# Kernel optimization log

Hardware: AMD Instinct MI355X
Metric: run time of the kernel (lower is better)

## Reference

```python
import jax, jax.numpy as jnp
import numpy as np

B = 65536
H = W = 28
K = 3
OUT_HW = H - K + 1  # 26, valid conv
FEAT = OUT_HW * OUT_HW  # 676
HID = 200
NCLS = 10


def setup_inputs() -> dict:
    key = jax.random.key(0)
    ks = jax.random.split(key, 6)
    x = jax.random.normal(ks[0], (B, H * W), dtype=jnp.float32)
    conv_w = jnp.ones((K, K), dtype=jnp.float32)  # Parameter(ones((3,3)))
    w1 = jax.random.normal(ks[1], (FEAT, HID), dtype=jnp.float32) * (1.0 / np.sqrt(FEAT))
    b1 = jnp.zeros((HID,), dtype=jnp.float32)
    w2 = jax.random.normal(ks[2], (HID, NCLS), dtype=jnp.float32) * (1.0 / np.sqrt(HID))
    b2 = jnp.zeros((NCLS,), dtype=jnp.float32)
    return {"x": x, "conv_w": conv_w, "w1": w1, "b1": b1, "w2": w2, "b2": b2}


def _forward(x, conv_w, w1, b1, w2, b2):
    img = x.reshape(-1, H, W)  # (B,28,28)
    # valid 3x3 single-channel cross-correlation (matches input[i:i+3,j:j+3]*w)
    lhs = img[:, None, :, :]          # (B,1,28,28)
    rhs = conv_w[None, None, :, :]    # (1,1,3,3)
    conv = jax.lax.conv_general_dilated(
        lhs, rhs, window_strides=(1, 1), padding="VALID",
        dimension_numbers=("NCHW", "OIHW", "NCHW"))  # (B,1,26,26)
    feat = conv.reshape(-1, FEAT)     # (B,676)
    hidden = jax.nn.relu(feat @ w1 + b1)  # (B,200)
    return hidden @ w2 + b2               # (B,10) logits


def reference(x, conv_w, w1, b1, w2, b2):
    return _forward(x, conv_w, w1, b1, w2, b2)
```

## Files before the change

### kernel.cpp

```cpp
#include <hip/hip_runtime.h>
#include <hip/hip_bf16.h>

#define BATCH   65536
#define HW      28
#define OHW     26
#define FEAT    676
#define HID     200
#define NCLS    10
#define MT      16
#define NBLOCKS (BATCH / MT)

typedef __attribute__((ext_vector_type(8))) __bf16 bf16x8;
typedef __attribute__((ext_vector_type(4))) float  f32x4;

__device__ __forceinline__ unsigned int pk2(float a, float b) {
  __hip_bfloat16 ha = __float2bfloat16(a), hb = __float2bfloat16(b);
  return (unsigned int)__builtin_bit_cast(unsigned short, ha)
       | ((unsigned int)__builtin_bit_cast(unsigned short, hb) << 16);
}

__device__ __forceinline__ unsigned short* fslot(unsigned short* base, int m, int k) {
  const int kc = k >> 5;
  return base + ((kc * 64 + ((k >> 3) & 3) * 16 + (m ^ (kc & 7))) * 8) + (k & 7);
}

__global__ __launch_bounds__(256) void prep_w1tf(const float* __restrict__ w1,
                                                 unsigned short* __restrict__ w1tf) {
  int idx = blockIdx.x * 256 + threadIdx.x;
  if (idx >= 704 * 208) return;
  int k = idx / 208;
  int n = idx - k * 208;
  float v = (k < FEAT && n < HID) ? w1[k * HID + n] : 0.f;
  int nt = n >> 4, ln = n & 15;
  int kc = k >> 5, r = k & 31, qd = r >> 3, j = r & 7;
  size_t dst = ((size_t)(kc * 13 + nt) * 64 + qd * 16 + ln) * 8 + j;
  __hip_bfloat16 h = __float2bfloat16(v);
  w1tf[dst] = __builtin_bit_cast(unsigned short, h);
}

__global__ __launch_bounds__(256) void prep_w2f(const float* __restrict__ w2,
                                                unsigned short* __restrict__ w2f) {
  int t = blockIdx.x * 256 + threadIdx.x;
  if (t >= 7 * 64 * 8) return;
  int j = t & 7, lane = (t >> 3) & 63, kc = t >> 9;
  int c = lane & 15;
  int k = kc * 32 + (lane >> 4) * 8 + j;
  float v = (c < NCLS && k < HID) ? w2[k * NCLS + c] : 0.f;
  __hip_bfloat16 h = __float2bfloat16(v);
  w2f[t] = __builtin_bit_cast(unsigned short, h);
}

template<int NT0, int NT>
__device__ __forceinline__ void gemm1_slice(
    const unsigned short* featA, const unsigned short* __restrict__ w1tf,
    const float* __restrict__ b1, unsigned short* hidA, int lane) {
  const int ln = lane & 15, qd = lane >> 4;
  f32x4 acc[NT];
  #pragma unroll
  for (int t = 0; t < NT; ++t) acc[t] = (f32x4){0.f, 0.f, 0.f, 0.f};
  for (int kc = 0; kc < 22; ++kc) {
    bf16x8 a = *(const bf16x8*)&featA[(kc * 64 + (lane ^ (kc & 7))) * 8];
    #pragma unroll
    for (int t = 0; t < NT; ++t) {
      bf16x8 b = *(const bf16x8*)(w1tf + ((size_t)(kc * 13 + NT0 + t) * 64 + lane) * 8);
      acc[t] = __builtin_amdgcn_mfma_f32_16x16x32_bf16(a, b, acc[t], 0, 0, 0);
    }
  }
  #pragma unroll
  for (int t = 0; t < NT; ++t) {
    const int n = (NT0 + t) * 16 + ln;
    if (n < HID) {
      const float bias = b1[n];
      const int kc2 = n >> 5, qd2 = (n >> 3) & 3, j2 = n & 7, c2 = kc2 & 7;
      #pragma unroll
      for (int rr = 0; rr < 4; ++rr) {
        const int m = qd * 4 + rr;
        float h = fmaxf(acc[t][rr] + bias, 0.f);
        __hip_bfloat16 hb = __float2bfloat16(h);
        hidA[(kc2 * 64 + qd2 * 16 + (m ^ c2)) * 8 + j2] =
            __builtin_bit_cast(unsigned short, hb);
      }
    }
  }
}

__global__ __launch_bounds__(256, 5) void fused2(
    const float* __restrict__ x, const float* __restrict__ cwp,
    const unsigned short* __restrict__ w1tf, const unsigned short* __restrict__ w2f,
    const float* __restrict__ b1, const float* __restrict__ b2,
    float* __restrict__ out) {
  __shared__ __align__(16) unsigned short featA[22 * 64 * 8];
  __shared__ __align__(16) unsigned short hidA [ 7 * 64 * 8];
  const int tid  = threadIdx.x;
  const int wave = tid >> 6;
  const int lane = tid & 63;

  for (int i = tid; i < MT * 14; i += 256) {
    int m = i / 14, d = i - m * 14;
    *(unsigned int*)fslot(featA, m, 676 + 2 * d) = 0u;
  }
  for (int i = tid; i < MT * 12; i += 256) {
    int m = i / 12, d = i - m * 12;
    *(unsigned int*)fslot(hidA, m, 200 + 2 * d) = 0u;
  }

  float cw[9];
  #pragma unroll
  for (int t = 0; t < 9; ++t) cw[t] = cwp[t];

  const float* xb = x + (size_t)blockIdx.x * (MT * 784);
  for (int t0 = 0; t0 < 364; t0 += 64) {
    const int t = t0 + lane;
    if (t < 364) {
      const int p   = (t * 721) >> 16;
      const int r91 = t - 91 * p;
      const int iq  = (r91 * 9363) >> 16;
      const int jc  = r91 - 7 * iq;
      const int m   = 4 * p + wave;
      const float* xw = xb + m * 784;
      float in[4][6];
      const int c2 = (jc < 6) ? 4 : 2;
      #pragma unroll
      for (int rr = 0; rr < 4; ++rr) {
        const float* rp = xw + (2 * iq + rr) * HW + 4 * jc;
        const float4 v = *(const float4*)rp;
        const float2 u = *(const float2*)(rp + c2);
        in[rr][0] = v.x; in[rr][1] = v.y; in[rr][2] = v.z; in[rr][3] = v.w;
        in[rr][4] = u.x; in[rr][5] = u.y;
      }
      float o[2][4];
      #pragma unroll
      for (int dr = 0; dr < 2; ++dr)
        #pragma unroll
        for (int dc = 0; dc < 4; ++dc) {
          float s = 0.f;
          #pragma unroll
          for (int di = 0; di < 3; ++di)
            #pragma unroll
            for (int dj = 0; dj < 3; ++dj)
              s += cw[di * 3 + dj] * in[dr + di][dc + dj];
          o[dr][dc] = s;
        }
      const int k0 = 52 * iq + 4 * jc;
      if (jc < 6) {
        *(uint2*)fslot(featA, m, k0) =
            make_uint2(pk2(o[0][0], o[0][1]), pk2(o[0][2], o[0][3]));
        *(unsigned int*)fslot(featA, m, k0 + OHW)     = pk2(o[1][0], o[1][1]);
        *(unsigned int*)fslot(featA, m, k0 + OHW + 2) = pk2(o[1][2], o[1][3]);
      } else {
        *(unsigned int*)fslot(featA, m, k0)       = pk2(o[0][0], o[0][1]);
        *(unsigned int*)fslot(featA, m, k0 + OHW) = pk2(o[1][0], o[1][1]);
      }
    }
  }
  __syncthreads();

  switch (wave) {
    case 0:  gemm1_slice<0, 4>(featA, w1tf, b1, hidA, lane); break;
    case 1:  gemm1_slice<4, 3>(featA, w1tf, b1, hidA, lane); break;
    case 2:  gemm1_slice<7, 3>(featA, w1tf, b1, hidA, lane); break;
    default: gemm1_slice<10, 3>(featA, w1tf, b1, hidA, lane); break;
  }
  __syncthreads();

  if (wave == 0) {
    const int ln = lane & 15, qd = lane >> 4;
    f32x4 acc2 = (f32x4){0.f, 0.f, 0.f, 0.f};
    #pragma unroll
    for (int kc = 0; kc < 7; ++kc) {
      bf16x8 a = *(const bf16x8*)&hidA[(kc * 64 + (lane ^ (kc & 7))) * 8];
      bf16x8 b = *(const bf16x8*)(w2f + ((size_t)kc * 64 + lane) * 8);
      acc2 = __builtin_amdgcn_mfma_f32_16x16x32_bf16(a, b, acc2, 0, 0, 0);
    }
    if (ln < NCLS) {
      const float bb = b2[ln];
      #pragma unroll
      for (int rr = 0; rr < 4; ++rr) {
        out[((size_t)blockIdx.x * MT + qd * 4 + rr) * NCLS + ln] = acc2[rr] + bb;
      }
    }
  }
}

extern "C" void kernel_launch(void* const* d_in, const int* in_sizes, int n_in,
                              void* d_out, int out_size, void* d_ws, size_t ws_size,
                              hipStream_t stream) {
  const float* x  = (const float*)d_in[0];
  const float* cw = (const float*)d_in[1];
  const float* w1 = (const float*)d_in[2];
  const float* b1 = (const float*)d_in[3];
  const float* w2 = (const float*)d_in[4];
  const float* b2 = (const float*)d_in[5];
  float* out = (float*)d_out;

  unsigned short* w1tf = (unsigned short*)d_ws;
  unsigned short* w2f  = (unsigned short*)((char*)d_ws + 294912);

  hipLaunchKernelGGL(prep_w1tf, dim3((704 * 208 + 255) / 256), dim3(256), 0, stream,
                     w1, w1tf);
  hipLaunchKernelGGL(prep_w2f, dim3(14), dim3(256), 0, stream, w2, w2f);
  hipLaunchKernelGGL(fused2, dim3(NBLOCKS), dim3(256), 0, stream,
                     x, cw, w1tf, w2f, b1, b2, out);
}
```

Before: 355.4 us.

## Split conv and GEMM into separate kernels with 64-row GEMM tiles

```diff
diff --git a/kernel.cpp b/kernel.cpp
--- a/kernel.cpp
+++ b/kernel.cpp
@@ -9,6 +9,8 @@
 #define NCLS    10
 #define MT      16
 #define NBLOCKS (BATCH / MT)
+#define MT2     64
+#define GBLOCKS (BATCH / MT2)
 
 typedef __attribute__((ext_vector_type(8))) __bf16 bf16x8;
 typedef __attribute__((ext_vector_type(4))) float  f32x4;
@@ -26,71 +28,45 @@
 
 __global__ __launch_bounds__(256) void prep_w1tf(const float* __restrict__ w1,
                                                  unsigned short* __restrict__ w1tf) {
-  int idx = blockIdx.x * 256 + threadIdx.x;
-  if (idx >= 704 * 208) return;
-  int k = idx / 208;
-  int n = idx - k * 208;
-  float v = (k < FEAT && n < HID) ? w1[k * HID + n] : 0.f;
-  int nt = n >> 4, ln = n & 15;
-  int kc = k >> 5, r = k & 31, qd = r >> 3, j = r & 7;
-  size_t dst = ((size_t)(kc * 13 + nt) * 64 + qd * 16 + ln) * 8 + j;
-  __hip_bfloat16 h = __float2bfloat16(v);
-  w1tf[dst] = __builtin_bit_cast(unsigned short, h);
+  int c = blockIdx.x * 256 + threadIdx.x;
+  if (c >= 22 * 13 * 64) return;
+  int ln = c & 15;
+  int qd = (c >> 4) & 3;
+  int g  = c >> 6;
+  int kc = g / 13, nt = g - kc * 13;
+  int n  = nt * 16 + ln;
+  float v[8];
+  #pragma unroll
+  for (int j = 0; j < 8; ++j) {
+    int k = kc * 32 + qd * 8 + j;
+    v[j] = (k < FEAT && n < HID) ? w1[k * HID + n] : 0.f;
+  }
+  uint4 o = make_uint4(pk2(v[0], v[1]), pk2(v[2], v[3]),
+                       pk2(v[4], v[5]), pk2(v[6], v[7]));
+  *(uint4*)(w1tf + (size_t)c * 8) = o;
 }
 
 __global__ __launch_bounds__(256) void prep_w2f(const float* __restrict__ w2,
                                                 unsigned short* __restrict__ w2f) {
-  int t = blockIdx.x * 256 + threadIdx.x;
-  if (t >= 7 * 64 * 8) return;
-  int j = t & 7, lane = (t >> 3) & 63, kc = t >> 9;
-  int c = lane & 15;
-  int k = kc * 32 + (lane >> 4) * 8 + j;
-  float v = (c < NCLS && k < HID) ? w2[k * NCLS + c] : 0.f;
-  __hip_bfloat16 h = __float2bfloat16(v);
-  w2f[t] = __builtin_bit_cast(unsigned short, h);
-}
-
-template<int NT0, int NT>
-__device__ __forceinline__ void gemm1_slice(
-    const unsigned short* featA, const unsigned short* __restrict__ w1tf,
-    const float* __restrict__ b1, unsigned short* hidA, int lane) {
-  const int ln = lane & 15, qd = lane >> 4;
-  f32x4 acc[NT];
-  #pragma unroll
-  for (int t = 0; t < NT; ++t) acc[t] = (f32x4){0.f, 0.f, 0.f, 0.f};
-  for (int kc = 0; kc < 22; ++kc) {
-    bf16x8 a = *(const bf16x8*)&featA[(kc * 64 + (lane ^ (kc & 7))) * 8];
-    #pragma unroll
-    for (int t = 0; t < NT; ++t) {
-      bf16x8 b = *(const bf16x8*)(w1tf + ((size_t)(kc * 13 + NT0 + t) * 64 + lane) * 8);
-      acc[t] = __builtin_amdgcn_mfma_f32_16x16x32_bf16(a, b, acc[t], 0, 0, 0);
-    }
-  }
-  #pragma unroll
-  for (int t = 0; t < NT; ++t) {
-    const int n = (NT0 + t) * 16 + ln;
-    if (n < HID) {
-      const float bias = b1[n];
-      const int kc2 = n >> 5, qd2 = (n >> 3) & 3, j2 = n & 7, c2 = kc2 & 7;
-      #pragma unroll
-      for (int rr = 0; rr < 4; ++rr) {
-        const int m = qd * 4 + rr;
-        float h = fmaxf(acc[t][rr] + bias, 0.f);
-        __hip_bfloat16 hb = __float2bfloat16(h);
-        hidA[(kc2 * 64 + qd2 * 16 + (m ^ c2)) * 8 + j2] =
-            __builtin_bit_cast(unsigned short, hb);
-      }
-    }
-  }
-}
-
-__global__ __launch_bounds__(256, 5) void fused2(
-    const float* __restrict__ x, const float* __restrict__ cwp,
-    const unsigned short* __restrict__ w1tf, const unsigned short* __restrict__ w2f,
-    const float* __restrict__ b1, const float* __restrict__ b2,
-    float* __restrict__ out) {
+  int c = blockIdx.x * 256 + threadIdx.x;
+  if (c >= 7 * 64) return;
+  int lane = c & 63, kc = c >> 6;
+  int col = lane & 15;
+  float v[8];
+  #pragma unroll
+  for (int j = 0; j < 8; ++j) {
+    int k = kc * 32 + (lane >> 4) * 8 + j;
+    v[j] = (col < NCLS && k < HID) ? w2[k * NCLS + col] : 0.f;
+  }
+  uint4 o = make_uint4(pk2(v[0], v[1]), pk2(v[2], v[3]),
+                       pk2(v[4], v[5]), pk2(v[6], v[7]));
+  *(uint4*)(w2f + (size_t)c * 8) = o;
+}
+
+__global__ __launch_bounds__(256) void convk(const float* __restrict__ x,
+                                             const float* __restrict__ cwp,
+                                             unsigned short* __restrict__ featg) {
   __shared__ __align__(16) unsigned short featA[22 * 64 * 8];
-  __shared__ __align__(16) unsigned short hidA [ 7 * 64 * 8];
   const int tid  = threadIdx.x;
   const int wave = tid >> 6;
   const int lane = tid & 63;
@@ -98,10 +74,6 @@
   for (int i = tid; i < MT * 14; i += 256) {
     int m = i / 14, d = i - m * 14;
     *(unsigned int*)fslot(featA, m, 676 + 2 * d) = 0u;
-  }
-  for (int i = tid; i < MT * 12; i += 256) {
-    int m = i / 12, d = i - m * 12;
-    *(unsigned int*)fslot(hidA, m, 200 + 2 * d) = 0u;
   }
 
   float cw[9];
@@ -155,6 +127,204 @@
   }
   __syncthreads();
 
+  const uint4* src = (const uint4*)featA;
+  uint4* dst = (uint4*)(featg + (size_t)blockIdx.x * (22 * 64 * 8));
+  for (int i = tid; i < 1408; i += 256) dst[i] = src[i];
+}
+
+template<int NT0, int NT>
+__device__ __forceinline__ void gemmB_slice(
+    const unsigned short* __restrict__ featg, const unsigned short* __restrict__ w1tf,
+    const float* __restrict__ b1, unsigned short* hidA, int lane, int blk4) {
+  const int ln = lane & 15, qd = lane >> 4;
+  f32x4 acc[4][NT];
+  #pragma unroll
+  for (int mi = 0; mi < 4; ++mi)
+    #pragma unroll
+    for (int t = 0; t < NT; ++t) acc[mi][t] = (f32x4){0.f, 0.f, 0.f, 0.f};
+
+  for (int kc = 0; kc < 22; ++kc) {
+    const int sw = lane ^ (kc & 7);
+    bf16x8 b[NT];
+    #pragma unroll
+    for (int t = 0; t < NT; ++t)
+      b[t] = *(const bf16x8*)(w1tf + ((size_t)(kc * 13 + NT0 + t) * 64 + lane) * 8);
+    bf16x8 a[4];
+    #pragma unroll
+    for (int mi = 0; mi < 4; ++mi)
+      a[mi] = *(const bf16x8*)(featg + ((size_t)((blk4 + mi) * 22 + kc) * 64 + sw) * 8);
+    #pragma unroll
+    for (int mi = 0; mi < 4; ++mi)
+      #pragma unroll
+      for (int t = 0; t < NT; ++t)
+        acc[mi][t] = __builtin_amdgcn_mfma_f32_16x16x32_bf16(a[mi], b[t], acc[mi][t], 0, 0, 0);
+  }
+
+  #pragma unroll
+  for (int t = 0; t < NT; ++t) {
+    const int n = (NT0 + t) * 16 + ln;
+    if (n < HID) {
+      const float bias = b1[n];
+      const int kc2 = n >> 5, qd2 = (n >> 3) & 3, j2 = n & 7, c2 = kc2 & 7;
+      #pragma unroll
+      for (int mi = 0; mi < 4; ++mi)
+        #pragma unroll
+        for (int rr = 0; rr < 4; ++rr) {
+          const int m = qd * 4 + rr;
+          float h = fmaxf(acc[mi][t][rr] + bias, 0.f);
+          __hip_bfloat16 hb = __float2bfloat16(h);
+          hidA[mi * 3584 + (kc2 * 64 + qd2 * 16 + (m ^ c2)) * 8 + j2] =
+              __builtin_bit_cast(unsigned short, hb);
+        }
+    }
+  }
+}
+
+__global__ __launch_bounds__(256, 4) void gemmk(
+    const unsigned short* __restrict__ featg, const unsigned short* __restrict__ w1tf,
+    const unsigned short* __restrict__ w2f, const float* __restrict__ b1,
+    const float* __restrict__ b2, float* __restrict__ out) {
+  __shared__ __align__(16) unsigned short hidA[4 * 7 * 64 * 8];
+  const int tid  = threadIdx.x;
+  const int wave = tid >> 6;
+  const int lane = tid & 63;
+
+  for (int i = tid; i < 768; i += 256) {
+    int mi = i / 192, r = i - mi * 192, m = r / 12, d = r - m * 12;
+    *(unsigned int*)fslot(hidA + mi * 3584, m, 200 + 2 * d) = 0u;
+  }
+
+  const int blk4 = blockIdx.x * 4;
+  switch (wave) {
+    case 0:  gemmB_slice<0, 4>(featg, w1tf, b1, hidA, lane, blk4); break;
+    case 1:  gemmB_slice<4, 3>(featg, w1tf, b1, hidA, lane, blk4); break;
+    case 2:  gemmB_slice<7, 3>(featg, w1tf, b1, hidA, lane, blk4); break;
+    default: gemmB_slice<10, 3>(featg, w1tf, b1, hidA, lane, blk4); break;
+  }
+  __syncthreads();
+
+  const int ln = lane & 15, qd = lane >> 4;
+  f32x4 acc2 = (f32x4){0.f, 0.f, 0.f, 0.f};
+  #pragma unroll
+  for (int kc = 0; kc < 7; ++kc) {
+    bf16x8 a = *(const bf16x8*)&hidA[wave * 3584 + (kc * 64 + (lane ^ (kc & 7))) * 8];
+    bf16x8 b = *(const bf16x8*)(w2f + ((size_t)kc * 64 + lane) * 8);
+    acc2 = __builtin_amdgcn_mfma_f32_16x16x32_bf16(a, b, acc2, 0, 0, 0);
+  }
+  if (ln < NCLS) {
+    const float bb = b2[ln];
+    #pragma unroll
+    for (int rr = 0; rr < 4; ++rr) {
+      out[((size_t)(blk4 + wave) * 16 + qd * 4 + rr) * NCLS + ln] = acc2[rr] + bb;
+    }
+  }
+}
+
+template<int NT0, int NT>
+__device__ __forceinline__ void gemm1_slice(
+    const unsigned short* featA, const unsigned short* __restrict__ w1tf,
+    const float* __restrict__ b1, unsigned short* hidA, int lane) {
+  const int ln = lane & 15, qd = lane >> 4;
+  f32x4 acc[NT];
+  #pragma unroll
+  for (int t = 0; t < NT; ++t) acc[t] = (f32x4){0.f, 0.f, 0.f, 0.f};
+  for (int kc = 0; kc < 22; ++kc) {
+    bf16x8 a = *(const bf16x8*)&featA[(kc * 64 + (lane ^ (kc & 7))) * 8];
+    #pragma unroll
+    for (int t = 0; t < NT; ++t) {
+      bf16x8 b = *(const bf16x8*)(w1tf + ((size_t)(kc * 13 + NT0 + t) * 64 + lane) * 8);
+      acc[t] = __builtin_amdgcn_mfma_f32_16x16x32_bf16(a, b, acc[t], 0, 0, 0);
+    }
+  }
+  #pragma unroll
+  for (int t = 0; t < NT; ++t) {
+    const int n = (NT0 + t) * 16 + ln;
+    if (n < HID) {
+      const float bias = b1[n];
+      const int kc2 = n >> 5, qd2 = (n >> 3) & 3, j2 = n & 7, c2 = kc2 & 7;
+      #pragma unroll
+      for (int rr = 0; rr < 4; ++rr) {
+        const int m = qd * 4 + rr;
+        float h = fmaxf(acc[t][rr] + bias, 0.f);
+        __hip_bfloat16 hb = __float2bfloat16(h);
+        hidA[(kc2 * 64 + qd2 * 16 + (m ^ c2)) * 8 + j2] =
+            __builtin_bit_cast(unsigned short, hb);
+      }
+    }
+  }
+}
+
+__global__ __launch_bounds__(256, 5) void fused2(
+    const float* __restrict__ x, const float* __restrict__ cwp,
+    const unsigned short* __restrict__ w1tf, const unsigned short* __restrict__ w2f,
+    const float* __restrict__ b1, const float* __restrict__ b2,
+    float* __restrict__ out) {
+  __shared__ __align__(16) unsigned short featA[22 * 64 * 8];
+  __shared__ __align__(16) unsigned short hidA [ 7 * 64 * 8];
+  const int tid  = threadIdx.x;
+  const int wave = tid >> 6;
+  const int lane = tid & 63;
+
+  for (int i = tid; i < MT * 14; i += 256) {
+    int m = i / 14, d = i - m * 14;
+    *(unsigned int*)fslot(featA, m, 676 + 2 * d) = 0u;
+  }
+  for (int i = tid; i < MT * 12; i += 256) {
+    int m = i / 12, d = i - m * 12;
+    *(unsigned int*)fslot(hidA, m, 200 + 2 * d) = 0u;
+  }
+
+  float cw[9];
+  #pragma unroll
+  for (int t = 0; t < 9; ++t) cw[t] = cwp[t];
+
+  const float* xb = x + (size_t)blockIdx.x * (MT * 784);
+  for (int t0 = 0; t0 < 364; t0 += 64) {
+    const int t = t0 + lane;
+    if (t < 364) {
+      const int p   = (t * 721) >> 16;
+      const int r91 = t - 91 * p;
+      const int iq  = (r91 * 9363) >> 16;
+      const int jc  = r91 - 7 * iq;
+      const int m   = 4 * p + wave;
+      const float* xw = xb + m * 784;
+      float in[4][6];
+      const int c2 = (jc < 6) ? 4 : 2;
+      #pragma unroll
+      for (int rr = 0; rr < 4; ++rr) {
+        const float* rp = xw + (2 * iq + rr) * HW + 4 * jc;
+        const float4 v = *(const float4*)rp;
+        const float2 u = *(const float2*)(rp + c2);
+        in[rr][0] = v.x; in[rr][1] = v.y; in[rr][2] = v.z; in[rr][3] = v.w;
+        in[rr][4] = u.x; in[rr][5] = u.y;
+      }
+      float o[2][4];
+      #pragma unroll
+      for (int dr = 0; dr < 2; ++dr)
+        #pragma unroll
+        for (int dc = 0; dc < 4; ++dc) {
+          float s = 0.f;
+          #pragma unroll
+          for (int di = 0; di < 3; ++di)
+            #pragma unroll
+            for (int dj = 0; dj < 3; ++dj)
+              s += cw[di * 3 + dj] * in[dr + di][dc + dj];
+          o[dr][dc] = s;
+        }
+      const int k0 = 52 * iq + 4 * jc;
+      if (jc < 6) {
+        *(uint2*)fslot(featA, m, k0) =
+            make_uint2(pk2(o[0][0], o[0][1]), pk2(o[0][2], o[0][3]));
+        *(unsigned int*)fslot(featA, m, k0 + OHW)     = pk2(o[1][0], o[1][1]);
+        *(unsigned int*)fslot(featA, m, k0 + OHW + 2) = pk2(o[1][2], o[1][3]);
+      } else {
+        *(unsigned int*)fslot(featA, m, k0)       = pk2(o[0][0], o[0][1]);
+        *(unsigned int*)fslot(featA, m, k0 + OHW) = pk2(o[1][0], o[1][1]);
+      }
+    }
+  }
+  __syncthreads();
+
   switch (wave) {
     case 0:  gemm1_slice<0, 4>(featA, w1tf, b1, hidA, lane); break;
     case 1:  gemm1_slice<4, 3>(featA, w1tf, b1, hidA, lane); break;
@@ -195,10 +365,19 @@
 
   unsigned short* w1tf = (unsigned short*)d_ws;
   unsigned short* w2f  = (unsigned short*)((char*)d_ws + 294912);
-
-  hipLaunchKernelGGL(prep_w1tf, dim3((704 * 208 + 255) / 256), dim3(256), 0, stream,
+  unsigned short* featg = (unsigned short*)((char*)d_ws + 307200);
+
+  hipLaunchKernelGGL(prep_w1tf, dim3((22 * 13 * 64 + 255) / 256), dim3(256), 0, stream,
                      w1, w1tf);
-  hipLaunchKernelGGL(prep_w2f, dim3(14), dim3(256), 0, stream, w2, w2f);
-  hipLaunchKernelGGL(fused2, dim3(NBLOCKS), dim3(256), 0, stream,
-                     x, cw, w1tf, w2f, b1, b2, out);
-}
+  hipLaunchKernelGGL(prep_w2f, dim3(2), dim3(256), 0, stream, w2, w2f);
+
+  const size_t need = 307200 + (size_t)NBLOCKS * 22528;
+  if (ws_size >= need) {
+    hipLaunchKernelGGL(convk, dim3(NBLOCKS), dim3(256), 0, stream, x, cw, featg);
+    hipLaunchKernelGGL(gemmk, dim3(GBLOCKS), dim3(256), 0, stream,
+                       featg, w1tf, w2f, b1, b2, out);
+  } else {
+    hipLaunchKernelGGL(fused2, dim3(NBLOCKS), dim3(256), 0, stream,
+                       x, cw, w1tf, w2f, b1, b2, out);
+  }
+}
```

Result: slower. 371.2 us (+4.4%).

## Rewrite conv stage as row-streaming with lane shuffles; vectorize weight prep

Applied to the files above, without the earlier changes.

```diff
diff --git a/kernel.cpp b/kernel.cpp
--- a/kernel.cpp
+++ b/kernel.cpp
@@ -26,28 +26,39 @@
 
 __global__ __launch_bounds__(256) void prep_w1tf(const float* __restrict__ w1,
                                                  unsigned short* __restrict__ w1tf) {
-  int idx = blockIdx.x * 256 + threadIdx.x;
-  if (idx >= 704 * 208) return;
-  int k = idx / 208;
-  int n = idx - k * 208;
-  float v = (k < FEAT && n < HID) ? w1[k * HID + n] : 0.f;
-  int nt = n >> 4, ln = n & 15;
-  int kc = k >> 5, r = k & 31, qd = r >> 3, j = r & 7;
-  size_t dst = ((size_t)(kc * 13 + nt) * 64 + qd * 16 + ln) * 8 + j;
-  __hip_bfloat16 h = __float2bfloat16(v);
-  w1tf[dst] = __builtin_bit_cast(unsigned short, h);
+  int c = blockIdx.x * 256 + threadIdx.x;
+  if (c >= 22 * 13 * 64) return;
+  int ln = c & 15;
+  int qd = (c >> 4) & 3;
+  int g  = c >> 6;
+  int kc = g / 13, nt = g - kc * 13;
+  int n  = nt * 16 + ln;
+  float v[8];
+  #pragma unroll
+  for (int j = 0; j < 8; ++j) {
+    int k = kc * 32 + qd * 8 + j;
+    v[j] = (k < FEAT && n < HID) ? w1[k * HID + n] : 0.f;
+  }
+  uint4 o = make_uint4(pk2(v[0], v[1]), pk2(v[2], v[3]),
+                       pk2(v[4], v[5]), pk2(v[6], v[7]));
+  *(uint4*)(w1tf + (size_t)c * 8) = o;
 }
 
 __global__ __launch_bounds__(256) void prep_w2f(const float* __restrict__ w2,
                                                 unsigned short* __restrict__ w2f) {
-  int t = blockIdx.x * 256 + threadIdx.x;
-  if (t >= 7 * 64 * 8) return;
-  int j = t & 7, lane = (t >> 3) & 63, kc = t >> 9;
-  int c = lane & 15;
-  int k = kc * 32 + (lane >> 4) * 8 + j;
-  float v = (c < NCLS && k < HID) ? w2[k * NCLS + c] : 0.f;
-  __hip_bfloat16 h = __float2bfloat16(v);
-  w2f[t] = __builtin_bit_cast(unsigned short, h);
+  int c = blockIdx.x * 256 + threadIdx.x;
+  if (c >= 7 * 64) return;
+  int lane = c & 63, kc = c >> 6;
+  int col = lane & 15;
+  float v[8];
+  #pragma unroll
+  for (int j = 0; j < 8; ++j) {
+    int k = kc * 32 + (lane >> 4) * 8 + j;
+    v[j] = (col < NCLS && k < HID) ? w2[k * NCLS + col] : 0.f;
+  }
+  uint4 o = make_uint4(pk2(v[0], v[1]), pk2(v[2], v[3]),
+                       pk2(v[4], v[5]), pk2(v[6], v[7]));
+  *(uint4*)(w2f + (size_t)c * 8) = o;
 }
 
 template<int NT0, int NT>
@@ -84,7 +95,7 @@
   }
 }
 
-__global__ __launch_bounds__(256, 5) void fused2(
+__global__ __launch_bounds__(256, 5) void fused3(
     const float* __restrict__ x, const float* __restrict__ cwp,
     const unsigned short* __restrict__ w1tf, const unsigned short* __restrict__ w2f,
     const float* __restrict__ b1, const float* __restrict__ b2,
@@ -109,48 +120,29 @@
   for (int t = 0; t < 9; ++t) cw[t] = cwp[t];
 
   const float* xb = x + (size_t)blockIdx.x * (MT * 784);
-  for (int t0 = 0; t0 < 364; t0 += 64) {
-    const int t = t0 + lane;
-    if (t < 364) {
-      const int p   = (t * 721) >> 16;
-      const int r91 = t - 91 * p;
-      const int iq  = (r91 * 9363) >> 16;
-      const int jc  = r91 - 7 * iq;
-      const int m   = 4 * p + wave;
-      const float* xw = xb + m * 784;
-      float in[4][6];
-      const int c2 = (jc < 6) ? 4 : 2;
-      #pragma unroll
-      for (int rr = 0; rr < 4; ++rr) {
-        const float* rp = xw + (2 * iq + rr) * HW + 4 * jc;
-        const float4 v = *(const float4*)rp;
-        const float2 u = *(const float2*)(rp + c2);
-        in[rr][0] = v.x; in[rr][1] = v.y; in[rr][2] = v.z; in[rr][3] = v.w;
-        in[rr][4] = u.x; in[rr][5] = u.y;
+  const int c  = lane & 31;
+  const int mi = lane >> 5;
+  const int cl = (c < 28) ? c : 27;
+  #pragma unroll
+  for (int q = 0; q < 2; ++q) {
+    const int m = wave * 4 + q * 2 + mi;
+    const float* xw = xb + m * 784;
+    float a0 = 0.f, a1 = 0.f;
+    #pragma unroll
+    for (int r = 0; r < 28; ++r) {
+      const float v  = xw[r * HW + cl];
+      const float v1 = __shfl(v, lane + 1, 64);
+      const float v2 = __shfl(v, lane + 2, 64);
+      const float t0 = cw[0] * v + cw[1] * v1 + cw[2] * v2;
+      const float t1 = cw[3] * v + cw[4] * v1 + cw[5] * v2;
+      const float t2 = cw[6] * v + cw[7] * v1 + cw[8] * v2;
+      if (r >= 2 && c < OHW) {
+        const float o = a1 + t2;
+        __hip_bfloat16 hb = __float2bfloat16(o);
+        *fslot(featA, m, (r - 2) * OHW + c) = __builtin_bit_cast(unsigned short, hb);
       }
-      float o[2][4];
-      #pragma unroll
-      for (int dr = 0; dr < 2; ++dr)
-        #pragma unroll
-        for (int dc = 0; dc < 4; ++dc) {
-          float s = 0.f;
-          #pragma unroll
-          for (int di = 0; di < 3; ++di)
-            #pragma unroll
-            for (int dj = 0; dj < 3; ++dj)
-              s += cw[di * 3 + dj] * in[dr + di][dc + dj];
-          o[dr][dc] = s;
-        }
-      const int k0 = 52 * iq + 4 * jc;
-      if (jc < 6) {
-        *(uint2*)fslot(featA, m, k0) =
-            make_uint2(pk2(o[0][0], o[0][1]), pk2(o[0][2], o[0][3]));
-        *(unsigned int*)fslot(featA, m, k0 + OHW)     = pk2(o[1][0], o[1][1]);
-        *(unsigned int*)fslot(featA, m, k0 + OHW + 2) = pk2(o[1][2], o[1][3]);
-      } else {
-        *(unsigned int*)fslot(featA, m, k0)       = pk2(o[0][0], o[0][1]);
-        *(unsigned int*)fslot(featA, m, k0 + OHW) = pk2(o[1][0], o[1][1]);
-      }
+      a1 = a0 + t1;
+      a0 = t0;
     }
   }
   __syncthreads();
@@ -196,9 +188,9 @@
   unsigned short* w1tf = (unsigned short*)d_ws;
   unsigned short* w2f  = (unsigned short*)((char*)d_ws + 294912);
 
-  hipLaunchKernelGGL(prep_w1tf, dim3((704 * 208 + 255) / 256), dim3(256), 0, stream,
+  hipLaunchKernelGGL(prep_w1tf, dim3((22 * 13 * 64 + 255) / 256), dim3(256), 0, stream,
                      w1, w1tf);
-  hipLaunchKernelGGL(prep_w2f, dim3(14), dim3(256), 0, stream, w2, w2f);
-  hipLaunchKernelGGL(fused2, dim3(NBLOCKS), dim3(256), 0, stream,
+  hipLaunchKernelGGL(prep_w2f, dim3(2), dim3(256), 0, stream, w2, w2f);
+  hipLaunchKernelGGL(fused3, dim3(NBLOCKS), dim3(256), 0, stream,
                      x, cw, w1tf, w2f, b1, b2, out);
 }
```

After: 403.8 us. 13.6% more time.
